# Optimization experiments

Hardware: AMD Instinct MI355X
Metric: run time of the kernel (lower is better)

The kernel has to match this reference:

```python
import jax, jax.numpy as jnp
import numpy as np

D = 128   # latent_dim
H = 128   # mlp_hidden_dim
S = 2     # message_passing_steps
NM = 30000   # mesh nodes
NO = 2000    # obj nodes
EMM = 240000 # mesh->mesh edges
EMO = 60000  # mesh->obj edges


def _ln(h, g, b):
    m = jnp.mean(h, axis=-1, keepdims=True)
    v = jnp.mean((h - m) ** 2, axis=-1, keepdims=True)
    return (h - m) * jax.lax.rsqrt(v + 1e-5) * g + b


def _mlp_ln(h, W0, b0, W1, b1, W2, b2, g, bt):
    # build_mlp(in, [H]*2, out) + LayerNorm(out)
    h = jax.nn.relu(h @ W0 + b0)
    h = jax.nn.relu(h @ W1 + b1)
    h = h @ W2 + b2
    return _ln(h, g, bt)


def _edge_conv(x_src, x_dst, ei, ea, W0, b0, W1, b1, W2, b2, g, bt):
    # PyG source_to_target: x_j = src gather (ei[0]), x_i = dst gather (ei[1])
    xi = x_dst[ei[1]]
    xj = x_src[ei[0]]
    msg = _mlp_ln(jnp.concatenate([xi, xj, ea], axis=-1), W0, b0, W1, b1, W2, b2, g, bt)
    aggr = jax.ops.segment_sum(msg, ei[1], num_segments=x_dst.shape[0])
    return ea + msg, aggr  # residual on edge attr; aggr is sum of raw messages


def _node_conv(x, aggr, W0, b0, W1, b1, W2, b2, g, bt):
    return x + _mlp_ln(jnp.concatenate([x, aggr], axis=-1), W0, b0, W1, b1, W2, b2, g, bt)


def setup_inputs() -> dict:
    key = jax.random.key(0)
    ks = jax.random.split(key, 16)
    f = jnp.float32
    x_mesh = jax.random.normal(ks[0], (NM, D), f)
    x_obj = jax.random.normal(ks[1], (NO, D), f)
    ea_mm = jax.random.normal(ks[2], (EMM, D), f)
    ea_mo = jax.random.normal(ks[3], (EMO, D), f)
    ei_mm = jnp.stack([jax.random.randint(ks[4], (EMM,), 0, NM),
                       jax.random.randint(ks[5], (EMM,), 0, NM)]).astype(jnp.int32)
    ei_mo = jnp.stack([jax.random.randint(ks[6], (EMO,), 0, NM),
                       jax.random.randint(ks[7], (EMO,), 0, NO)]).astype(jnp.int32)

    def w(k, shape, fan):
        return jax.random.normal(k, shape, f) * (1.0 / np.sqrt(fan))

    # params stacked as [edge_or_node_type(2), step(S), ...]
    eW0 = w(ks[8], (2, S, 3 * D, H), 3 * D); eb0 = jnp.zeros((2, S, H), f)
    eW1 = w(ks[9], (2, S, H, H), H);         eb1 = jnp.zeros((2, S, H), f)
    eW2 = w(ks[10], (2, S, H, D), H);        eb2 = jnp.zeros((2, S, D), f)
    eg = jnp.ones((2, S, D), f);             ebt = jnp.zeros((2, S, D), f)
    nW0 = w(ks[11], (2, S, 2 * D, H), 2 * D); nb0 = jnp.zeros((2, S, H), f)
    nW1 = w(ks[12], (2, S, H, H), H);         nb1 = jnp.zeros((2, S, H), f)
    nW2 = w(ks[13], (2, S, H, D), H);         nb2 = jnp.zeros((2, S, D), f)
    ng = jnp.ones((2, S, D), f);              nbt = jnp.zeros((2, S, D), f)
    return dict(x_mesh=x_mesh, x_obj=x_obj, ei_mm=ei_mm, ei_mo=ei_mo,
                ea_mm=ea_mm, ea_mo=ea_mo,
                eW0=eW0, eb0=eb0, eW1=eW1, eb1=eb1, eW2=eW2, eb2=eb2, eg=eg, ebt=ebt,
                nW0=nW0, nb0=nb0, nW1=nW1, nb1=nb1, nW2=nW2, nb2=nb2, ng=ng, nbt=nbt)


def reference(x_mesh, x_obj, ei_mm, ei_mo, ea_mm, ea_mo,
              eW0, eb0, eW1, eb1, eW2, eb2, eg, ebt,
              nW0, nb0, nW1, nb1, nW2, nb2, ng, nbt):
    for s in range(S):
        ep = lambda t: (eW0[t, s], eb0[t, s], eW1[t, s], eb1[t, s], eW2[t, s], eb2[t, s], eg[t, s], ebt[t, s])
        npar = lambda t: (nW0[t, s], nb0[t, s], nW1[t, s], nb1[t, s], nW2[t, s], nb2[t, s], ng[t, s], nbt[t, s])
        # edge convs use node features at layer input
        ea_mm, agg_mesh = _edge_conv(x_mesh, x_mesh, ei_mm, ea_mm, *ep(0))
        ea_mo, agg_obj = _edge_conv(x_mesh, x_obj, ei_mo, ea_mo, *ep(1))
        x_mesh = _node_conv(x_mesh, agg_mesh, *npar(0))
        x_obj = _node_conv(x_obj, agg_obj, *npar(1))
    return (x_mesh, x_obj)
```

## Files before the change

kernel.cpp:

```cpp
#include <hip/hip_runtime.h>

#define DD 128
#define NMESH 30000
#define NOBJ 2000
#define EMMN 240000
#define EMON 60000

typedef unsigned short u16;
typedef short short8 __attribute__((ext_vector_type(8)));
typedef short short4v __attribute__((ext_vector_type(4)));
typedef float f32x4 __attribute__((ext_vector_type(4)));
typedef __bf16 bf16x8 __attribute__((ext_vector_type(8)));

union FragCvt { short8 s; bf16x8 b; };

static __device__ __forceinline__ u16 f2bf(float f) {
  union { float f; unsigned u; } v; v.f = f;
  unsigned r = v.u + 0x7FFFu + ((v.u >> 16) & 1u);
  return (u16)(r >> 16);
}
static __device__ __forceinline__ float bf2f(u16 u) {
  union { unsigned u; float f; } v; v.u = ((unsigned)u) << 16; return v.f;
}
static __device__ __forceinline__ int swz256(int row, int b) {
  return row * 256 + (b ^ ((row & 7) << 4));
}
static __device__ __forceinline__ bf16x8 ldsFrag(const u16* s, int row, int kByte) {
  FragCvt u; u.s = *(const short8*)((const char*)s + swz256(row, kByte));
  return u.b;
}

static __device__ __forceinline__ void stage_w(u16* sW, const u16* src, int rowLen, int colOff, int tid) {
  const int wrow = tid >> 1, wh = tid & 1;
  const u16* w = src + (size_t)wrow * rowLen + colOff + wh * 64;
  #pragma unroll
  for (int j = 0; j < 8; ++j) {
    short8 v = *(const short8*)(w + j * 8);
    *(short8*)((char*)sW + swz256(wrow, wh * 128 + j * 16)) = v;
  }
}

static __device__ __forceinline__ void mfma_128k(const u16* sIn, const u16* sW,
                                                 int wr, int wc, int lrow, int lk,
                                                 f32x4 acc[2][4]) {
  #pragma unroll
  for (int kc = 0; kc < 4; ++kc) {
    bf16x8 a0 = ldsFrag(sIn, wr * 32 + lrow, kc * 64 + lk * 16);
    bf16x8 a1 = ldsFrag(sIn, wr * 32 + 16 + lrow, kc * 64 + lk * 16);
    #pragma unroll
    for (int ct = 0; ct < 4; ++ct) {
      bf16x8 b = ldsFrag(sW, wc * 64 + ct * 16 + lrow, kc * 64 + lk * 16);
      acc[0][ct] = __builtin_amdgcn_mfma_f32_16x16x32_bf16(a0, b, acc[0][ct], 0, 0, 0);
      acc[1][ct] = __builtin_amdgcn_mfma_f32_16x16x32_bf16(a1, b, acc[1][ct], 0, 0, 0);
// ... 10 lines not shown
    for (int ct = 0; ct < 4; ++ct) {
      const int col = wc * 64 + ct * 16 + lrow;
      const float bias = sBias[biasOff + col];
      #pragma unroll
      for (int r = 0; r < 4; ++r) {
        const int orow = wr * 32 + rt * 16 + lk * 4 + r;
        float v = acc[rt][ct][r] + bias;
        v = fmaxf(v, 0.f);
        *(u16*)((char*)sIn + swz256(orow, col * 2)) = f2bf(v);
        acc[rt][ct][r] = 0.f;
      }
    }
  }
}

static __device__ __forceinline__ void store_h3(float* sH, const float* sBias,
                                                int wr, int wc, int lrow, int lk,
                                                f32x4 acc[2][4]) {
  #pragma unroll
  for (int rt = 0; rt < 2; ++rt) {
    #pragma unroll
    for (int ct = 0; ct < 4; ++ct) {
      const int col = wc * 64 + ct * 16 + lrow;
      const float bias = sBias[256 + col];
      #pragma unroll
      for (int r = 0; r < 4; ++r) {
        const int orow = wr * 32 + rt * 16 + lk * 4 + r;
        sH[orow * 132 + col] = acc[rt][ct][r] + bias;
      }
    }
  }
}

__global__ __launch_bounds__(256, 2) void edge_conv_kernel(
    const u16* __restrict__ xsrc, const u16* __restrict__ xdst,
    const int* __restrict__ ei, const int E,
    const float* __restrict__ ea_f32, u16* __restrict__ ea_bf,
    const u16* __restrict__ W0T, const u16* __restrict__ W1T, const u16* __restrict__ W2T,
    const float* __restrict__ b0, const float* __restrict__ b1, const float* __restrict__ b2,
    const float* __restrict__ gg, const float* __restrict__ btp,
    u16* __restrict__ msg_out)
{
  __shared__ u16 sIn[64 * 128];
  __shared__ __align__(16) char sWHraw[64 * 132 * 4];
  __shared__ float sBias[5 * 128];
  __shared__ int sIdx[128];
  u16* sW = (u16*)sWHraw;
  float* sH = (float*)sWHraw;

  const int tid = threadIdx.x;
  const int wave = tid >> 6, lane = tid & 63;
  const int lrow = lane & 15, lk = lane >> 4;
  const int wr = wave >> 1, wc = wave & 1;
  const int e0 = blockIdx.x * 64;
  const int row = tid >> 2, seg = tid & 3;

  if (tid < 128) {
    sBias[tid] = b0[tid];
    sBias[128 + tid] = b1[tid];
    sBias[256 + tid] = b2[tid];
    sBias[384 + tid] = gg[tid];
    sBias[512 + tid] = btp[tid];
  }
  if (tid < 64) {
    int e = e0 + tid; if (e >= E) e = E - 1;
    sIdx[tid] = ei[e];
    sIdx[64 + tid] = ei[E + e];
  }
  __syncthreads();

  const int eRow = (e0 + row < E) ? (e0 + row) : (E - 1);
  const f32x4 zero = {0.f, 0.f, 0.f, 0.f};
  f32x4 acc[2][4];
  #pragma unroll
  for (int i = 0; i < 2; ++i)
    #pragma unroll
    for (int j = 0; j < 4; ++j) acc[i][j] = zero;

  #pragma unroll
  for (int p = 0; p < 3; ++p) {
    if (p < 2) {
      const u16* xb = (p == 0) ? xdst : xsrc;
      const int idx = (p == 0) ? sIdx[64 + row] : sIdx[row];
      const u16* srow = xb + (size_t)idx * DD;
      #pragma unroll
      for (int j = 0; j < 4; ++j) {
        short8 v = *(const short8*)(srow + seg * 32 + j * 8);
        *(short8*)((char*)sIn + swz256(row, seg * 64 + j * 16)) = v;
      }
    } else if (ea_f32) {
      const float* er = ea_f32 + (size_t)eRow * DD;
      #pragma unroll
      for (int j = 0; j < 4; ++j) {
        const int c0 = seg * 32 + j * 8;
        f32x4 f0 = *(const f32x4*)(er + c0);
        f32x4 f1 = *(const f32x4*)(er + c0 + 4);
        short8 v;
        #pragma unroll
        for (int q = 0; q < 4; ++q) { v[q] = (short)f2bf(f0[q]); v[4 + q] = (short)f2bf(f1[q]); }
        *(short8*)((char*)sIn + swz256(row, seg * 64 + j * 16)) = v;
      }
    } else {
      const u16* er = ea_bf + (size_t)eRow * DD;
      #pragma unroll
      for (int j = 0; j < 4; ++j) {
        short8 v = *(const short8*)(er + seg * 32 + j * 8);
        *(short8*)((char*)sIn + swz256(row, seg * 64 + j * 16)) = v;
      }
    }
    stage_w(sW, W0T, 384, p * 128, tid);
    __syncthreads();
    mfma_128k(sIn, sW, wr, wc, lrow, lk, acc);
    __syncthreads();
  }

  transition_relu(sIn, sBias, 0, wr, wc, lrow, lk, acc);
  stage_w(sW, W1T, 128, 0, tid);
  __syncthreads();
  mfma_128k(sIn, sW, wr, wc, lrow, lk, acc);
  __syncthreads();

  transition_relu(sIn, sBias, 128, wr, wc, lrow, lk, acc);
  stage_w(sW, W2T, 128, 0, tid);
  __syncthreads();
  mfma_128k(sIn, sW, wr, wc, lrow, lk, acc);
  __syncthreads();

  store_h3(sH, sBias, wr, wc, lrow, lk, acc);
  __syncthreads();

  {
    const float* hrow = sH + row * 132 + seg * 32;
    f32x4 vv[8];
    float s1 = 0.f, s2 = 0.f;
    #pragma unroll
    for (int j = 0; j < 8; ++j) {
      vv[j] = *(const f32x4*)(hrow + j * 4);
      #pragma unroll
      for (int q = 0; q < 4; ++q) { s1 += vv[j][q]; s2 += vv[j][q] * vv[j][q]; }
    }
    s1 += __shfl_xor(s1, 1); s1 += __shfl_xor(s1, 2);
    s2 += __shfl_xor(s2, 1); s2 += __shfl_xor(s2, 2);
    const float m = s1 * (1.f / 128.f);
    const float var = s2 * (1.f / 128.f) - m * m;
    const float rstd = rsqrtf(var + 1e-5f);
    const int e = e0 + row;
    if (e < E) {
      u16* eaRow = ea_bf + (size_t)e * DD + seg * 32;
      u16* msgRow = msg_out + (size_t)e * DD + seg * 32;
      float eold[32];
      if (ea_f32) {
        const float* er = ea_f32 + (size_t)e * DD + seg * 32;
        #pragma unroll
        for (int j = 0; j < 8; ++j) {
          f32x4 t = *(const f32x4*)(er + j * 4);
          #pragma unroll
          for (int q = 0; q < 4; ++q) eold[j * 4 + q] = t[q];
        }
      } else {
        #pragma unroll
        for (int j4 = 0; j4 < 4; ++j4) {
          short8 t = *(const short8*)(eaRow + j4 * 8);
          #pragma unroll
          for (int q = 0; q < 8; ++q) eold[j4 * 8 + q] = bf2f((u16)t[q]);
        }
      }
      #pragma unroll
      for (int j4 = 0; j4 < 4; ++j4) {
        short8 en, ms;
        #pragma unroll
        for (int q = 0; q < 8; ++q) {
          const int cl = j4 * 8 + q;
          const int c = seg * 32 + cl;
          const float msg = (vv[cl >> 2][cl & 3] - m) * rstd * sBias[384 + c] + sBias[512 + c];
          en[q] = (short)f2bf(eold[cl] + msg);
          ms[q] = (short)f2bf(msg);
        }
        *(short8*)(eaRow + j4 * 8) = en;
        *(short8*)(msgRow + j4 * 8) = ms;
      }
    }
  }
}

__global__ void hist_kernel(const int* __restrict__ ei, int E, int* __restrict__ deg) {
  int i = blockIdx.x * blockDim.x + threadIdx.x;
  if (i < E) atomicAdd(&deg[ei[E + i]], 1);
}

__global__ __launch_bounds__(1024) void scan_kernel(const int* __restrict__ deg,
                                                    int* __restrict__ start,
                                                    int* __restrict__ cursor, int N) {
  __shared__ int lds[1024];
  const int t = threadIdx.x;
  const int chunk = (N + 1023) >> 10;
  const int base = t * chunk;
  const int end = min(base + chunk, N);
  int s = 0;
  for (int i = base; i < end; ++i) s += deg[i];
  lds[t] = s;
  __syncthreads();
  for (int d = 1; d < 1024; d <<= 1) {
    int v = (t >= d) ? lds[t - d] : 0;
    __syncthreads();
    lds[t] += v;
    __syncthreads();
  }
  int off = lds[t] - s;
  for (int i = base; i < end; ++i) { start[i] = off; cursor[i] = off; off += deg[i]; }
  if (t == 1023) start[N] = lds[1023];
}

__global__ void scatter_kernel(const int* __restrict__ ei, int E,
                               int* __restrict__ cursor, int* __restrict__ perm) {
  int i = blockIdx.x * blockDim.x + threadIdx.x;
  if (i < E) { int p = atomicAdd(&cursor[ei[E + i]], 1); perm[p] = i; }
}

__global__ __launch_bounds__(256) void agg_gather_kernel(
    const u16* __restrict__ msg, const int* __restrict__ start,
    const int* __restrict__ perm, float* __restrict__ agg, int N)
{
  const int wave = threadIdx.x >> 6, lane = threadIdx.x & 63;
  const int n = blockIdx.x * 4 + wave;
  if (n >= N) return;
  const int i0 = start[n], i1 = start[n + 1];
  float a0 = 0.f, a1 = 0.f;
  for (int i = i0; i < i1; ++i) {
    const int e = perm[i];
    unsigned v = *(const unsigned*)(msg + (size_t)e * DD + lane * 2);
    a0 += bf2f((u16)(v & 0xFFFFu));
    a1 += bf2f((u16)(v >> 16));
  }
  float* ar = agg + (size_t)n * DD + lane * 2;
  ar[0] = a0;
  ar[1] = a1;
}

__global__ __launch_bounds__(256, 2) void node_conv_kernel(
    u16* __restrict__ x_bf, const float* __restrict__ aggin,
    float* __restrict__ x_f32, const int N,
    const u16* __restrict__ W0T, const u16* __restrict__ W1T, const u16* __restrict__ W2T,
    const float* __restrict__ b0, const float* __restrict__ b1, const float* __restrict__ b2,
    const float* __restrict__ gg, const float* __restrict__ btp)
{
  __shared__ u16 sIn[64 * 128];
  __shared__ __align__(16) char sWHraw[64 * 132 * 4];
  __shared__ float sBias[5 * 128];
  u16* sW = (u16*)sWHraw;
  float* sH = (float*)sWHraw;

  const int tid = threadIdx.x;
  const int wave = tid >> 6, lane = tid & 63;
  const int lrow = lane & 15, lk = lane >> 4;
  const int wr = wave >> 1, wc = wave & 1;
  const int n0 = blockIdx.x * 64;
  const int row = tid >> 2, seg = tid & 3;
  const int nRow = (n0 + row < N) ? (n0 + row) : (N - 1);

  if (tid < 128) {
    sBias[tid] = b0[tid];
    sBias[128 + tid] = b1[tid];
    sBias[256 + tid] = b2[tid];
    sBias[384 + tid] = gg[tid];
    sBias[512 + tid] = btp[tid];
  }
  __syncthreads();

  const f32x4 zero = {0.f, 0.f, 0.f, 0.f};
  f32x4 acc[2][4];
  #pragma unroll
  for (int i = 0; i < 2; ++i)
    #pragma unroll
    for (int j = 0; j < 4; ++j) acc[i][j] = zero;

  {
    const u16* srow = x_bf + (size_t)nRow * DD;
    #pragma unroll
    for (int j = 0; j < 4; ++j) {
      short8 v = *(const short8*)(srow + seg * 32 + j * 8);
      *(short8*)((char*)sIn + swz256(row, seg * 64 + j * 16)) = v;
    }
    stage_w(sW, W0T, 256, 0, tid);
  }
  __syncthreads();
  mfma_128k(sIn, sW, wr, wc, lrow, lk, acc);
  __syncthreads();
  {
    const float* ar = aggin + (size_t)nRow * DD;
    #pragma unroll
    for (int j = 0; j < 4; ++j) {
      const int c0 = seg * 32 + j * 8;
      f32x4 f0 = *(const f32x4*)(ar + c0);
      f32x4 f1 = *(const f32x4*)(ar + c0 + 4);
      short8 v;
      #pragma unroll
      for (int q = 0; q < 4; ++q) { v[q] = (short)f2bf(f0[q]); v[4 + q] = (short)f2bf(f1[q]); }
      *(short8*)((char*)sIn + swz256(row, seg * 64 + j * 16)) = v;
    }
    stage_w(sW, W0T, 256, 128, tid);
  }
  __syncthreads();
  mfma_128k(sIn, sW, wr, wc, lrow, lk, acc);
  __syncthreads();

  transition_relu(sIn, sBias, 0, wr, wc, lrow, lk, acc);
  stage_w(sW, W1T, 128, 0, tid);
  __syncthreads();
  mfma_128k(sIn, sW, wr, wc, lrow, lk, acc);
  __syncthreads();

  transition_relu(sIn, sBias, 128, wr, wc, lrow, lk, acc);
  stage_w(sW, W2T, 128, 0, tid);
  __syncthreads();
  mfma_128k(sIn, sW, wr, wc, lrow, lk, acc);
  __syncthreads();

  store_h3(sH, sBias, wr, wc, lrow, lk, acc);
  __syncthreads();

  {
    const float* hrow = sH + row * 132 + seg * 32;
    f32x4 vv[8];
    float s1 = 0.f, s2 = 0.f;
    #pragma unroll
    for (int j = 0; j < 8; ++j) {
      vv[j] = *(const f32x4*)(hrow + j * 4);
      #pragma unroll
      for (int q = 0; q < 4; ++q) { s1 += vv[j][q]; s2 += vv[j][q] * vv[j][q]; }
    }
    s1 += __shfl_xor(s1, 1); s1 += __shfl_xor(s1, 2);
    s2 += __shfl_xor(s2, 1); s2 += __shfl_xor(s2, 2);
    const float m = s1 * (1.f / 128.f);
    const float var = s2 * (1.f / 128.f) - m * m;
    const float rstd = rsqrtf(var + 1e-5f);
    const int n = n0 + row;
    if (n < N) {
      float* xr = x_f32 + (size_t)n * DD + seg * 32;
      u16* xb = x_bf + (size_t)n * DD + seg * 32;
      #pragma unroll
      for (int j = 0; j < 8; ++j) {
        f32x4 xold = *(const f32x4*)(xr + j * 4);
        f32x4 nv;
        short4v pb;
        #pragma unroll
        for (int q = 0; q < 4; ++q) {
          const int c = seg * 32 + j * 4 + q;
          const float ln = (vv[j][q] - m) * rstd * sBias[384 + c] + sBias[512 + c];
          nv[q] = xold[q] + ln;
          pb[q] = (short)f2bf(nv[q]);
        }
        *(f32x4*)(xr + j * 4) = nv;
        *(short4v*)(xb + j * 4) = pb;
      }
    }
  }
}

__global__ void prep_w_kernel(const float* __restrict__ src, u16* __restrict__ dst, int K) {
  int i = blockIdx.x * blockDim.x + threadIdx.x;
  int total = 4 * K * 128;
  if (i < total) {
    int n = i & 127;
    int k = (i >> 7) % K;
    int sl = i / (K * 128);
    dst[((size_t)sl * 128 + n) * K + k] = f2bf(src[i]);
  }
}

__global__ void prep_x_kernel(const float* __restrict__ xm, const float* __restrict__ xo,
                              float* __restrict__ xf, u16* __restrict__ xmb, u16* __restrict__ xob) {
  int i = blockIdx.x * blockDim.x + threadIdx.x;
  const int tm = NMESH * DD;
  const int to = NOBJ * DD;
  if (i < tm) { float v = xm[i]; xf[i] = v; xmb[i] = f2bf(v); }
  else if (i < tm + to) { int j = i - tm; float v = xo[j]; xf[tm + j] = v; xob[j] = f2bf(v); }
}

extern "C" void kernel_launch(void* const* d_in, const int* in_sizes, int n_in,
                              void* d_out, int out_size, void* d_ws, size_t ws_size,
                              hipStream_t stream)
{
  const float* x_mesh = (const float*)d_in[0];
  const float* x_obj  = (const float*)d_in[1];
  const int*   ei_mm  = (const int*)d_in[2];
  const int*   ei_mo  = (const int*)d_in[3];
  const float* ea_mm  = (const float*)d_in[4];
  const float* ea_mo  = (const float*)d_in[5];
  const float* eW0 = (const float*)d_in[6];
  const float* eb0 = (const float*)d_in[7];
  const float* eW1 = (const float*)d_in[8];
// ... 25 lines not shown
  u16* nW2T = nW1T + (size_t)4 * 128 * 128;
  u16* msg_mm = nW2T + (size_t)4 * 128 * 128;
  u16* msg_mo = msg_mm + (size_t)EMMN * DD;
  int* deg_m   = (int*)(msg_mo + (size_t)EMON * DD);
  int* start_m = deg_m + NMESH;
  int* cur_m   = start_m + NMESH + 1;
  int* perm_mm = cur_m + NMESH;
  int* deg_o   = perm_mm + EMMN;
  int* start_o = deg_o + NOBJ;
  int* cur_o   = start_o + NOBJ + 1;
  int* perm_mo = cur_o + NOBJ;

  float* xf_m = (float*)d_out;
  float* xf_o = xf_m + (size_t)NMESH * DD;

  prep_w_kernel<<<768, 256, 0, stream>>>(eW0, eW0T, 384);
  prep_w_kernel<<<256, 256, 0, stream>>>(eW1, eW1T, 128);
  prep_w_kernel<<<256, 256, 0, stream>>>(eW2, eW2T, 128);
  prep_w_kernel<<<512, 256, 0, stream>>>(nW0, nW0T, 256);
  prep_w_kernel<<<256, 256, 0, stream>>>(nW1, nW1T, 128);
  prep_w_kernel<<<256, 256, 0, stream>>>(nW2, nW2T, 128);
  prep_x_kernel<<<16000, 256, 0, stream>>>(x_mesh, x_obj, xf_m, xm_bf, xo_bf);

  hipMemsetAsync(deg_m, 0, NMESH * sizeof(int), stream);
  hipMemsetAsync(deg_o, 0, NOBJ * sizeof(int), stream);
  hist_kernel<<<(EMMN + 255) / 256, 256, 0, stream>>>(ei_mm, EMMN, deg_m);
  hist_kernel<<<(EMON + 255) / 256, 256, 0, stream>>>(ei_mo, EMON, deg_o);
  scan_kernel<<<1, 1024, 0, stream>>>(deg_m, start_m, cur_m, NMESH);
  scan_kernel<<<1, 1024, 0, stream>>>(deg_o, start_o, cur_o, NOBJ);
  scatter_kernel<<<(EMMN + 255) / 256, 256, 0, stream>>>(ei_mm, EMMN, cur_m, perm_mm);
  scatter_kernel<<<(EMON + 255) / 256, 256, 0, stream>>>(ei_mo, EMON, cur_o, perm_mo);

  for (int s = 0; s < 2; ++s) {
    {
      int sl = 0 * 2 + s;
      edge_conv_kernel<<<EMMN / 64, 256, 0, stream>>>(
          xm_bf, xm_bf, ei_mm, EMMN,
          (s == 0) ? ea_mm : (const float*)nullptr, eamm_bf,
          eW0T + (size_t)sl * 128 * 384, eW1T + (size_t)sl * 128 * 128, eW2T + (size_t)sl * 128 * 128,
          eb0 + sl * 128, eb1 + sl * 128, eb2 + sl * 128, eg + sl * 128, ebt + sl * 128,
          msg_mm);
    }
    {
      int sl = 1 * 2 + s;
      edge_conv_kernel<<<(EMON + 63) / 64, 256, 0, stream>>>(
          xm_bf, xo_bf, ei_mo, EMON,
          (s == 0) ? ea_mo : (const float*)nullptr, eamo_bf,
          eW0T + (size_t)sl * 128 * 384, eW1T + (size_t)sl * 128 * 128, eW2T + (size_t)sl * 128 * 128,
          eb0 + sl * 128, eb1 + sl * 128, eb2 + sl * 128, eg + sl * 128, ebt + sl * 128,
          msg_mo);
    }
    agg_gather_kernel<<<(NMESH + 3) / 4, 256, 0, stream>>>(msg_mm, start_m, perm_mm, agg_m, NMESH);
    agg_gather_kernel<<<(NOBJ + 3) / 4, 256, 0, stream>>>(msg_mo, start_o, perm_mo, agg_o, NOBJ);
    {
      int sl = 0 * 2 + s;
      node_conv_kernel<<<(NMESH + 63) / 64, 256, 0, stream>>>(
          xm_bf, agg_m, xf_m, NMESH,
          nW0T + (size_t)sl * 128 * 256, nW1T + (size_t)sl * 128 * 128, nW2T + (size_t)sl * 128 * 128,
          nb0 + sl * 128, nb1 + sl * 128, nb2 + sl * 128, ng + sl * 128, nbt + sl * 128);
    }
    {
      int sl = 1 * 2 + s;
      node_conv_kernel<<<(NOBJ + 63) / 64, 256, 0, stream>>>(
          xo_bf, agg_o, xf_o, NOBJ,
          nW0T + (size_t)sl * 128 * 256, nW1T + (size_t)sl * 128 * 128, nW2T + (size_t)sl * 128 * 128,
          nb0 + sl * 128, nb1 + sl * 128, nb2 + sl * 128, ng + sl * 128, nbt + sl * 128);
    }
  }
}
```

Baseline: 683.5 us.

## Merge per-type launches, enlarge tiles, async weight staging, register LayerNorm

Mesh-mesh and mesh-obj edge convs now run in one launch, as do the two node convs and the aggregation gathers. Prep, histogram, scan and scatter are also merged into fewer kernels, which cuts launch count and tail effects. Tiles grow from 64 to 128 rows with 512 threads, and weights are staged into LDS with async global_load_lds. LayerNorm is computed from accumulators in registers via a cross-wave partial-sum exchange, replacing the fp32 shared-memory round trip, and output stores use nontemporal hints. The larger shared footprint and different occupancy could cost latency hiding.

```diff
diff --git a/kernel.cpp b/kernel.cpp
--- a/kernel.cpp
+++ b/kernel.cpp
@@ -5,10 +5,13 @@
 #define NOBJ 2000
 #define EMMN 240000
 #define EMON 60000
+#define NB_MM (EMMN / 128)
+#define NB_MO ((EMON + 127) / 128)
+#define NB_NM ((NMESH + 127) / 128)
+#define NB_NO ((NOBJ + 127) / 128)
 
 typedef unsigned short u16;
 typedef short short8 __attribute__((ext_vector_type(8)));
-typedef short short4v __attribute__((ext_vector_type(4)));
 typedef float f32x4 __attribute__((ext_vector_type(4)));
 typedef __bf16 bf16x8 __attribute__((ext_vector_type(8)));
 
@@ -30,13 +33,21 @@
   return u.b;
 }
 
-static __device__ __forceinline__ void stage_w(u16* sW, const u16* src, int rowLen, int colOff, int tid) {
-  const int wrow = tid >> 1, wh = tid & 1;
-  const u16* w = src + (size_t)wrow * rowLen + colOff + wh * 64;
-  #pragma unroll
-  for (int j = 0; j < 8; ++j) {
-    short8 v = *(const short8*)(w + j * 8);
-    *(short8*)((char*)sW + swz256(wrow, wh * 128 + j * 16)) = v;
+static __device__ __forceinline__ void gload_lds16(const void* g, void* l) {
+  __builtin_amdgcn_global_load_lds((const __attribute__((address_space(1))) void*)g,
+                                   (__attribute__((address_space(3))) void*)l, 16, 0, 0);
+}
+
+static __device__ __forceinline__ void stage_w_async(u16* sW, const u16* W,
+                                                     int rowLen, int colOff, int tid) {
+  const int w = tid >> 6, lane = tid & 63;
+  #pragma unroll
+  for (int j = 0; j < 4; ++j) {
+    const int base_row = (j * 8 + w) * 4;
+    const int row = base_row + (lane >> 4);
+    const int chunk = (lane & 15) ^ (row & 7);
+    const u16* g = W + (size_t)row * rowLen + colOff + chunk * 8;
+    gload_lds16(g, (char*)sW + base_row * 256);
   }
 }
 
@@ -77,62 +88,108 @@
   }
 }
 
-static __device__ __forceinline__ void store_h3(float* sH, const float* sBias,
-                                                int wr, int wc, int lrow, int lk,
-                                                f32x4 acc[2][4]) {
+static __device__ __forceinline__ void ln_to_sIn(u16* sIn, float* sPart, const float* sBias,
+                                                 int wr, int wc, int lrow, int lk,
+                                                 f32x4 acc[2][4]) {
+  float gv[4], bv[4];
+  #pragma unroll
+  for (int ct = 0; ct < 4; ++ct) {
+    const int col = wc * 64 + ct * 16 + lrow;
+    gv[ct] = sBias[384 + col];
+    bv[ct] = sBias[512 + col];
+  }
+  float s1[2][4], s2[2][4];
   #pragma unroll
   for (int rt = 0; rt < 2; ++rt) {
     #pragma unroll
-    for (int ct = 0; ct < 4; ++ct) {
-      const int col = wc * 64 + ct * 16 + lrow;
-      const float bias = sBias[256 + col];
+    for (int r = 0; r < 4; ++r) {
+      float a = 0.f, b = 0.f;
+      #pragma unroll
+      for (int ct = 0; ct < 4; ++ct) {
+        const int col = wc * 64 + ct * 16 + lrow;
+        const float v = acc[rt][ct][r] + sBias[256 + col];
+        acc[rt][ct][r] = v;
+        a += v; b += v * v;
+      }
+      #pragma unroll
+      for (int m = 1; m < 16; m <<= 1) { a += __shfl_xor(a, m); b += __shfl_xor(b, m); }
+      s1[rt][r] = a; s2[rt][r] = b;
+    }
+  }
+  if (lrow == 0) {
+    #pragma unroll
+    for (int rt = 0; rt < 2; ++rt)
       #pragma unroll
       for (int r = 0; r < 4; ++r) {
-        const int orow = wr * 32 + rt * 16 + lk * 4 + r;
-        sH[orow * 132 + col] = acc[rt][ct][r] + bias;
+        const int e = wr * 32 + rt * 16 + lk * 4 + r;
+        sPart[(wc * 128 + e) * 2] = s1[rt][r];
+        sPart[(wc * 128 + e) * 2 + 1] = s2[rt][r];
+      }
+  }
+  __syncthreads();
+  #pragma unroll
+  for (int rt = 0; rt < 2; ++rt)
+    #pragma unroll
+    for (int r = 0; r < 4; ++r) {
+      const int e = wr * 32 + rt * 16 + lk * 4 + r;
+      const float t1 = s1[rt][r] + sPart[((1 - wc) * 128 + e) * 2];
+      const float t2 = s2[rt][r] + sPart[((1 - wc) * 128 + e) * 2 + 1];
+      const float m = t1 * (1.f / 128.f);
+      const float var = t2 * (1.f / 128.f) - m * m;
+      const float rstd = rsqrtf(var + 1e-5f);
+      #pragma unroll
+      for (int ct = 0; ct < 4; ++ct) {
+        const int col = wc * 64 + ct * 16 + lrow;
+        const float ln = (acc[rt][ct][r] - m) * rstd * gv[ct] + bv[ct];
+        *(u16*)((char*)sIn + swz256(e, col * 2)) = f2bf(ln);
       }
     }
-  }
-}
-
-__global__ __launch_bounds__(256, 2) void edge_conv_kernel(
-    const u16* __restrict__ xsrc, const u16* __restrict__ xdst,
-    const int* __restrict__ ei, const int E,
-    const float* __restrict__ ea_f32, u16* __restrict__ ea_bf,
-    const u16* __restrict__ W0T, const u16* __restrict__ W1T, const u16* __restrict__ W2T,
-    const float* __restrict__ b0, const float* __restrict__ b1, const float* __restrict__ b2,
-    const float* __restrict__ gg, const float* __restrict__ btp,
-    u16* __restrict__ msg_out)
-{
-  __shared__ u16 sIn[64 * 128];
-  __shared__ __align__(16) char sWHraw[64 * 132 * 4];
-  __shared__ float sBias[5 * 128];
-  __shared__ int sIdx[128];
-  u16* sW = (u16*)sWHraw;
-  float* sH = (float*)sWHraw;
-
+}
+
+static __device__ __forceinline__ void stage_rows_bf(u16* sIn, const u16* src, int row, int seg) {
+  #pragma unroll
+  for (int j = 0; j < 4; ++j) {
+    short8 v = *(const short8*)(src + seg * 32 + j * 8);
+    *(short8*)((char*)sIn + swz256(row, seg * 64 + j * 16)) = v;
+  }
+}
+static __device__ __forceinline__ void stage_rows_f32(u16* sIn, const float* src, int row, int seg) {
+  #pragma unroll
+  for (int j = 0; j < 4; ++j) {
+    const int c0 = seg * 32 + j * 8;
+    f32x4 f0 = *(const f32x4*)(src + c0);
+    f32x4 f1 = *(const f32x4*)(src + c0 + 4);
+    short8 v;
+    #pragma unroll
+    for (int q = 0; q < 4; ++q) { v[q] = (short)f2bf(f0[q]); v[4 + q] = (short)f2bf(f1[q]); }
+    *(short8*)((char*)sIn + swz256(row, seg * 64 + j * 16)) = v;
+  }
+}
+
+static __device__ void edge_body(int bid,
+    const u16* xsrc, const u16* xdst, const int* ei, int E,
+    const float* ea_f32, u16* ea_bf,
+    const u16* W0T, const u16* W1T, const u16* W2T,
+    const float* b0, const float* b1, const float* b2,
+    const float* gq, const float* btq, u16* msg_out,
+    u16* sIn, u16* sW, float* sBias, float* sPart)
+{
   const int tid = threadIdx.x;
   const int wave = tid >> 6, lane = tid & 63;
   const int lrow = lane & 15, lk = lane >> 4;
   const int wr = wave >> 1, wc = wave & 1;
-  const int e0 = blockIdx.x * 64;
+  const int e0 = bid * 128;
   const int row = tid >> 2, seg = tid & 3;
+  const int eRow = (e0 + row < E) ? (e0 + row) : (E - 1);
 
   if (tid < 128) {
     sBias[tid] = b0[tid];
     sBias[128 + tid] = b1[tid];
     sBias[256 + tid] = b2[tid];
-    sBias[384 + tid] = gg[tid];
-    sBias[512 + tid] = btp[tid];
-  }
-  if (tid < 64) {
-    int e = e0 + tid; if (e >= E) e = E - 1;
-    sIdx[tid] = ei[e];
-    sIdx[64 + tid] = ei[E + e];
-  }
-  __syncthreads();
-
-  const int eRow = (e0 + row < E) ? (e0 + row) : (E - 1);
+    sBias[384 + tid] = gq[tid];
+    sBias[512 + tid] = btq[tid];
+  }
+
   const f32x4 zero = {0.f, 0.f, 0.f, 0.f};
   f32x4 acc[2][4];
   #pragma unroll
@@ -140,120 +197,223 @@
     #pragma unroll
     for (int j = 0; j < 4; ++j) acc[i][j] = zero;
 
-  #pragma unroll
-  for (int p = 0; p < 3; ++p) {
-    if (p < 2) {
-      const u16* xb = (p == 0) ? xdst : xsrc;
-      const int idx = (p == 0) ? sIdx[64 + row] : sIdx[row];
-      const u16* srow = xb + (size_t)idx * DD;
+  stage_w_async(sW, W0T, 384, 0, tid);
+  { const int idx = ei[E + eRow]; stage_rows_bf(sIn, xdst + (size_t)idx * DD, row, seg); }
+  __syncthreads();
+  mfma_128k(sIn, sW, wr, wc, lrow, lk, acc);
+  __syncthreads();
+
+  stage_w_async(sW, W0T, 384, 128, tid);
+  { const int idx = ei[eRow]; stage_rows_bf(sIn, xsrc + (size_t)idx * DD, row, seg); }
+  __syncthreads();
+  mfma_128k(sIn, sW, wr, wc, lrow, lk, acc);
+  __syncthreads();
+
+  stage_w_async(sW, W0T, 384, 256, tid);
+  if (ea_f32) stage_rows_f32(sIn, ea_f32 + (size_t)eRow * DD, row, seg);
+  else        stage_rows_bf(sIn, ea_bf + (size_t)eRow * DD, row, seg);
+  __syncthreads();
+  mfma_128k(sIn, sW, wr, wc, lrow, lk, acc);
+  __syncthreads();
+
+  transition_relu(sIn, sBias, 0, wr, wc, lrow, lk, acc);
+  stage_w_async(sW, W1T, 128, 0, tid);
+  __syncthreads();
+  mfma_128k(sIn, sW, wr, wc, lrow, lk, acc);
+  __syncthreads();
+
+  transition_relu(sIn, sBias, 128, wr, wc, lrow, lk, acc);
+  stage_w_async(sW, W2T, 128, 0, tid);
+  __syncthreads();
+  mfma_128k(sIn, sW, wr, wc, lrow, lk, acc);
+  __syncthreads();
+
+  ln_to_sIn(sIn, sPart, sBias, wr, wc, lrow, lk, acc);
+  __syncthreads();
+
+  const int e = e0 + row;
+  if (e < E) {
+    short8 msgv[4];
+    #pragma unroll
+    for (int j = 0; j < 4; ++j)
+      msgv[j] = *(const short8*)((const char*)sIn + swz256(row, seg * 64 + j * 16));
+    u16* msgRow = msg_out + (size_t)e * DD + seg * 32;
+    u16* eaRow  = ea_bf + (size_t)e * DD + seg * 32;
+    if (ea_f32) {
+      const float* er = ea_f32 + (size_t)e * DD + seg * 32;
       #pragma unroll
       for (int j = 0; j < 4; ++j) {
-        short8 v = *(const short8*)(srow + seg * 32 + j * 8);
-        *(short8*)((char*)sIn + swz256(row, seg * 64 + j * 16)) = v;
-      }
-    } else if (ea_f32) {
-      const float* er = ea_f32 + (size_t)eRow * DD;
+        f32x4 o0 = __builtin_nontemporal_load((const f32x4*)(er + j * 8));
+        f32x4 o1 = __builtin_nontemporal_load((const f32x4*)(er + j * 8 + 4));
+        short8 en;
+        #pragma unroll
+        for (int q = 0; q < 4; ++q) {
+          en[q]     = (short)f2bf(o0[q] + bf2f((u16)msgv[j][q]));
+          en[4 + q] = (short)f2bf(o1[q] + bf2f((u16)msgv[j][4 + q]));
+        }
+        __builtin_nontemporal_store(en, (short8*)(eaRow + j * 8));
+        __builtin_nontemporal_store(msgv[j], (short8*)(msgRow + j * 8));
+      }
+    } else {
       #pragma unroll
       for (int j = 0; j < 4; ++j) {
-        const int c0 = seg * 32 + j * 8;
-        f32x4 f0 = *(const f32x4*)(er + c0);
-        f32x4 f1 = *(const f32x4*)(er + c0 + 4);
-        short8 v;
+        short8 old = __builtin_nontemporal_load((const short8*)(eaRow + j * 8));
+        short8 en;
         #pragma unroll
-        for (int q = 0; q < 4; ++q) { v[q] = (short)f2bf(f0[q]); v[4 + q] = (short)f2bf(f1[q]); }
-        *(short8*)((char*)sIn + swz256(row, seg * 64 + j * 16)) = v;
-      }
-    } else {
-      const u16* er = ea_bf + (size_t)eRow * DD;
-      #pragma unroll
-      for (int j = 0; j < 4; ++j) {
-        short8 v = *(const short8*)(er + seg * 32 + j * 8);
-        *(short8*)((char*)sIn + swz256(row, seg * 64 + j * 16)) = v;
+        for (int q = 0; q < 8; ++q)
+          en[q] = (short)f2bf(bf2f((u16)old[q]) + bf2f((u16)msgv[j][q]));
+        __builtin_nontemporal_store(en, (short8*)(eaRow + j * 8));
+        __builtin_nontemporal_store(msgv[j], (short8*)(msgRow + j * 8));
       }
     }
-    stage_w(sW, W0T, 384, p * 128, tid);
-    __syncthreads();
-    mfma_128k(sIn, sW, wr, wc, lrow, lk, acc);
-    __syncthreads();
-  }
+  }
+}
+
+__global__ __launch_bounds__(512, 4) void edge_conv_kernel(
+    const u16* __restrict__ xm_bf, const u16* __restrict__ xo_bf,
+    const int* __restrict__ ei_mm, const int* __restrict__ ei_mo,
+    const float* __restrict__ eaf_mm, const float* __restrict__ eaf_mo,
+    u16* __restrict__ eab_mm, u16* __restrict__ eab_mo,
+    const u16* __restrict__ W0a, const u16* __restrict__ W1a, const u16* __restrict__ W2a,
+    const u16* __restrict__ W0b, const u16* __restrict__ W1b, const u16* __restrict__ W2b,
+    const float* __restrict__ b0a, const float* __restrict__ b1a, const float* __restrict__ b2a,
+    const float* __restrict__ ga, const float* __restrict__ bta,
+    const float* __restrict__ b0b, const float* __restrict__ b1b, const float* __restrict__ b2b,
+    const float* __restrict__ gb, const float* __restrict__ btb,
+    u16* __restrict__ msg_mm, u16* __restrict__ msg_mo)
+{
+  __shared__ u16 sIn[128 * 128];
+  __shared__ u16 sW[128 * 128];
+  __shared__ float sBias[5 * 128];
+  __shared__ float sPart[2 * 128 * 2];
+  if ((int)blockIdx.x < NB_MM)
+    edge_body(blockIdx.x, xm_bf, xm_bf, ei_mm, EMMN, eaf_mm, eab_mm,
+              W0a, W1a, W2a, b0a, b1a, b2a, ga, bta, msg_mm, sIn, sW, sBias, sPart);
+  else
+    edge_body(blockIdx.x - NB_MM, xm_bf, xo_bf, ei_mo, EMON, eaf_mo, eab_mo,
+              W0b, W1b, W2b, b0b, b1b, b2b, gb, btb, msg_mo, sIn, sW, sBias, sPart);
+}
+
+static __device__ void node_body(int bid, u16* x_bf, const float* aggin, float* x_f32, int N,
+    const u16* W0T, const u16* W1T, const u16* W2T,
+    const float* b0, const float* b1, const float* b2,
+    const float* gq, const float* btq,
+    u16* sIn, u16* sW, float* sBias, float* sPart)
+{
+  const int tid = threadIdx.x;
+  const int wave = tid >> 6, lane = tid & 63;
+  const int lrow = lane & 15, lk = lane >> 4;
+  const int wr = wave >> 1, wc = wave & 1;
+  const int n0 = bid * 128;
+  const int row = tid >> 2, seg = tid & 3;
+  const int nRow = (n0 + row < N) ? (n0 + row) : (N - 1);
+
+  if (tid < 128) {
+    sBias[tid] = b0[tid];
+    sBias[128 + tid] = b1[tid];
+    sBias[256 + tid] = b2[tid];
+    sBias[384 + tid] = gq[tid];
+    sBias[512 + tid] = btq[tid];
+  }
+
+  const f32x4 zero = {0.f, 0.f, 0.f, 0.f};
+  f32x4 acc[2][4];
+  #pragma unroll
+  for (int i = 0; i < 2; ++i)
+    #pragma unroll
+    for (int j = 0; j < 4; ++j) acc[i][j] = zero;
+
+  stage_w_async(sW, W0T, 256, 0, tid);
+  stage_rows_bf(sIn, x_bf + (size_t)nRow * DD, row, seg);
+  __syncthreads();
+  mfma_128k(sIn, sW, wr, wc, lrow, lk, acc);
+  __syncthreads();
+
+  stage_w_async(sW, W0T, 256, 128, tid);
+  stage_rows_f32(sIn, aggin + (size_t)nRow * DD, row, seg);
+  __syncthreads();
+  mfma_128k(sIn, sW, wr, wc, lrow, lk, acc);
+  __syncthreads();
 
   transition_relu(sIn, sBias, 0, wr, wc, lrow, lk, acc);
-  stage_w(sW, W1T, 128, 0, tid);
+  stage_w_async(sW, W1T, 128, 0, tid);
   __syncthreads();
   mfma_128k(sIn, sW, wr, wc, lrow, lk, acc);
   __syncthreads();
 
   transition_relu(sIn, sBias, 128, wr, wc, lrow, lk, acc);
-  stage_w(sW, W2T, 128, 0, tid);
-  __syncthreads();
-  mfma_128k(sIn, sW, wr, wc, lrow, lk, acc);
-  __syncthreads();
-
-  store_h3(sH, sBias, wr, wc, lrow, lk, acc);
-  __syncthreads();
-
-  {
-    const float* hrow = sH + row * 132 + seg * 32;
-    f32x4 vv[8];
-    float s1 = 0.f, s2 = 0.f;
-    #pragma unroll
-    for (int j = 0; j < 8; ++j) {
-      vv[j] = *(const f32x4*)(hrow + j * 4);
-      #pragma unroll
-      for (int q = 0; q < 4; ++q) { s1 += vv[j][q]; s2 += vv[j][q] * vv[j][q]; }
+  stage_w_async(sW, W2T, 128, 0, tid);
+  __syncthreads();
+  mfma_128k(sIn, sW, wr, wc, lrow, lk, acc);
+  __syncthreads();
+
+  ln_to_sIn(sIn, sPart, sBias, wr, wc, lrow, lk, acc);
+  __syncthreads();
+
+  const int n = n0 + row;
+  if (n < N) {
+    short8 lnv[4];
+    #pragma unroll
+    for (int j = 0; j < 4; ++j)
+      lnv[j] = *(const short8*)((const char*)sIn + swz256(row, seg * 64 + j * 16));
+    float* xr = x_f32 + (size_t)n * DD + seg * 32;
+    u16* xb = x_bf + (size_t)n * DD + seg * 32;
+    #pragma unroll
+    for (int j = 0; j < 4; ++j) {
+      f32x4 o0 = *(const f32x4*)(xr + j * 8);
+      f32x4 o1 = *(const f32x4*)(xr + j * 8 + 4);
+      f32x4 n0v, n1v;
+      short8 pb;
+      #pragma unroll
+      for (int q = 0; q < 4; ++q) {
+        n0v[q] = o0[q] + bf2f((u16)lnv[j][q]);
+        n1v[q] = o1[q] + bf2f((u16)lnv[j][4 + q]);
+        pb[q]     = (short)f2bf(n0v[q]);
+        pb[4 + q] = (short)f2bf(n1v[q]);
+      }
+      *(f32x4*)(xr + j * 8) = n0v;
+      *(f32x4*)(xr + j * 8 + 4) = n1v;
+      *(short8*)(xb + j * 8) = pb;
     }
-    s1 += __shfl_xor(s1, 1); s1 += __shfl_xor(s1, 2);
-    s2 += __shfl_xor(s2, 1); s2 += __shfl_xor(s2, 2);
-    const float m = s1 * (1.f / 128.f);
-    const float var = s2 * (1.f / 128.f) - m * m;
-    const float rstd = rsqrtf(var + 1e-5f);
-    const int e = e0 + row;
-    if (e < E) {
-      u16* eaRow = ea_bf + (size_t)e * DD + seg * 32;
-      u16* msgRow = msg_out + (size_t)e * DD + seg * 32;
-      float eold[32];
-      if (ea_f32) {
-        const float* er = ea_f32 + (size_t)e * DD + seg * 32;
-        #pragma unroll
-        for (int j = 0; j < 8; ++j) {
-          f32x4 t = *(const f32x4*)(er + j * 4);
-          #pragma unroll
-          for (int q = 0; q < 4; ++q) eold[j * 4 + q] = t[q];
-        }
-      } else {
-        #pragma unroll
-        for (int j4 = 0; j4 < 4; ++j4) {
-          short8 t = *(const short8*)(eaRow + j4 * 8);
-          #pragma unroll
-          for (int q = 0; q < 8; ++q) eold[j4 * 8 + q] = bf2f((u16)t[q]);
-        }
-      }
-      #pragma unroll
-      for (int j4 = 0; j4 < 4; ++j4) {
-        short8 en, ms;
-        #pragma unroll
-        for (int q = 0; q < 8; ++q) {
-          const int cl = j4 * 8 + q;
-          const int c = seg * 32 + cl;
-          const float msg = (vv[cl >> 2][cl & 3] - m) * rstd * sBias[384 + c] + sBias[512 + c];
-          en[q] = (short)f2bf(eold[cl] + msg);
-          ms[q] = (short)f2bf(msg);
-        }
-        *(short8*)(eaRow + j4 * 8) = en;
-        *(short8*)(msgRow + j4 * 8) = ms;
-      }
-    }
-  }
-}
-
-__global__ void hist_kernel(const int* __restrict__ ei, int E, int* __restrict__ deg) {
+  }
+}
+
+__global__ __launch_bounds__(512, 4) void node_conv_kernel(
+    u16* __restrict__ xm_bf, u16* __restrict__ xo_bf,
+    const float* __restrict__ agg_m, const float* __restrict__ agg_o,
+    float* __restrict__ xf_m, float* __restrict__ xf_o,
+    const u16* __restrict__ W0a, const u16* __restrict__ W1a, const u16* __restrict__ W2a,
+    const u16* __restrict__ W0b, const u16* __restrict__ W1b, const u16* __restrict__ W2b,
+    const float* __restrict__ b0a, const float* __restrict__ b1a, const float* __restrict__ b2a,
+    const float* __restrict__ ga, const float* __restrict__ bta,
+    const float* __restrict__ b0b, const float* __restrict__ b1b, const float* __restrict__ b2b,
+    const float* __restrict__ gb, const float* __restrict__ btb)
+{
+  __shared__ u16 sIn[128 * 128];
+  __shared__ u16 sW[128 * 128];
+  __shared__ float sBias[5 * 128];
+  __shared__ float sPart[2 * 128 * 2];
+  if ((int)blockIdx.x < NB_NM)
+    node_body(blockIdx.x, xm_bf, agg_m, xf_m, NMESH,
+              W0a, W1a, W2a, b0a, b1a, b2a, ga, bta, sIn, sW, sBias, sPart);
+  else
+    node_body(blockIdx.x - NB_NM, xo_bf, agg_o, xf_o, NOBJ,
+              W0b, W1b, W2b, b0b, b1b, b2b, gb, btb, sIn, sW, sBias, sPart);
+}
+
+__global__ void hist_kernel(const int* __restrict__ ei_mm, const int* __restrict__ ei_mo,
+                            int* __restrict__ deg_m, int* __restrict__ deg_o) {
   int i = blockIdx.x * blockDim.x + threadIdx.x;
-  if (i < E) atomicAdd(&deg[ei[E + i]], 1);
-}
-
-__global__ __launch_bounds__(1024) void scan_kernel(const int* __restrict__ deg,
-                                                    int* __restrict__ start,
-                                                    int* __restrict__ cursor, int N) {
+  if (i < EMMN) atomicAdd(&deg_m[ei_mm[EMMN + i]], 1);
+  else { int j = i - EMMN; if (j < EMON) atomicAdd(&deg_o[ei_mo[EMON + j]], 1); }
+}
+
+__global__ __launch_bounds__(1024) void scan_kernel(
+    const int* __restrict__ deg_m, int* __restrict__ start_m, int* __restrict__ cur_m,
+    const int* __restrict__ deg_o, int* __restrict__ start_o, int* __restrict__ cur_o) {
+  const int* deg; int* start; int* cursor; int N;
+  if (blockIdx.x == 0) { deg = deg_m; start = start_m; cursor = cur_m; N = NMESH; }
+  else                 { deg = deg_o; start = start_o; cursor = cur_o; N = NOBJ; }
   __shared__ int lds[1024];
   const int t = threadIdx.x;
   const int chunk = (N + 1023) >> 10;
@@ -274,170 +434,84 @@
   if (t == 1023) start[N] = lds[1023];
 }
 
-__global__ void scatter_kernel(const int* __restrict__ ei, int E,
-                               int* __restrict__ cursor, int* __restrict__ perm) {
+__global__ void scatter_kernel(const int* __restrict__ ei_mm, const int* __restrict__ ei_mo,
+                               int* __restrict__ cur_m, int* __restrict__ cur_o,
+                               int* __restrict__ perm_m, int* __restrict__ perm_o) {
   int i = blockIdx.x * blockDim.x + threadIdx.x;
-  if (i < E) { int p = atomicAdd(&cursor[ei[E + i]], 1); perm[p] = i; }
+  if (i < EMMN) { int p = atomicAdd(&cur_m[ei_mm[EMMN + i]], 1); perm_m[p] = i; }
+  else { int j = i - EMMN; if (j < EMON) { int p = atomicAdd(&cur_o[ei_mo[EMON + j]], 1); perm_o[p] = j; } }
 }
 
 __global__ __launch_bounds__(256) void agg_gather_kernel(
-    const u16* __restrict__ msg, const int* __restrict__ start,
-    const int* __restrict__ perm, float* __restrict__ agg, int N)
+    const u16* __restrict__ msg_m, const int* __restrict__ start_m, const int* __restrict__ perm_m,
+    float* __restrict__ agg_m,
+    const u16* __restrict__ msg_o, const int* __restrict__ start_o, const int* __restrict__ perm_o,
+    float* __restrict__ agg_o)
 {
   const int wave = threadIdx.x >> 6, lane = threadIdx.x & 63;
-  const int n = blockIdx.x * 4 + wave;
-  if (n >= N) return;
+  int idx = blockIdx.x * 4 + wave;
+  const u16* msg; const int* start; const int* perm; float* agg; int n;
+  if (idx < NMESH) { msg = msg_m; start = start_m; perm = perm_m; agg = agg_m; n = idx; }
+  else {
+    n = idx - NMESH;
+    if (n >= NOBJ) return;
+    msg = msg_o; start = start_o; perm = perm_o; agg = agg_o;
+  }
   const int i0 = start[n], i1 = start[n + 1];
   float a0 = 0.f, a1 = 0.f;
-  for (int i = i0; i < i1; ++i) {
-    const int e = perm[i];
-    unsigned v = *(const unsigned*)(msg + (size_t)e * DD + lane * 2);
-    a0 += bf2f((u16)(v & 0xFFFFu));
-    a1 += bf2f((u16)(v >> 16));
+  int i = i0;
+  for (; i + 1 < i1; i += 2) {
+    const int e1 = perm[i], e2 = perm[i + 1];
+    unsigned v1 = __builtin_nontemporal_load((const unsigned*)(msg + (size_t)e1 * DD + lane * 2));
+    unsigned v2 = __builtin_nontemporal_load((const unsigned*)(msg + (size_t)e2 * DD + lane * 2));
+    a0 += bf2f((u16)(v1 & 0xFFFFu)) + bf2f((u16)(v2 & 0xFFFFu));
+    a1 += bf2f((u16)(v1 >> 16)) + bf2f((u16)(v2 >> 16));
+  }
+  if (i < i1) {
+    const int e1 = perm[i];
+    unsigned v1 = __builtin_nontemporal_load((const unsigned*)(msg + (size_t)e1 * DD + lane * 2));
+    a0 += bf2f((u16)(v1 & 0xFFFFu));
+    a1 += bf2f((u16)(v1 >> 16));
   }
   float* ar = agg + (size_t)n * DD + lane * 2;
   ar[0] = a0;
   ar[1] = a1;
 }
 
-__global__ __launch_bounds__(256, 2) void node_conv_kernel(
-    u16* __restrict__ x_bf, const float* __restrict__ aggin,
-    float* __restrict__ x_f32, const int N,
-    const u16* __restrict__ W0T, const u16* __restrict__ W1T, const u16* __restrict__ W2T,
-    const float* __restrict__ b0, const float* __restrict__ b1, const float* __restrict__ b2,
-    const float* __restrict__ gg, const float* __restrict__ btp)
-{
-  __shared__ u16 sIn[64 * 128];
-  __shared__ __align__(16) char sWHraw[64 * 132 * 4];
-  __shared__ float sBias[5 * 128];
-  u16* sW = (u16*)sWHraw;
-  float* sH = (float*)sWHraw;
-
-  const int tid = threadIdx.x;
-  const int wave = tid >> 6, lane = tid & 63;
-  const int lrow = lane & 15, lk = lane >> 4;
-  const int wr = wave >> 1, wc = wave & 1;
-  const int n0 = blockIdx.x * 64;
-  const int row = tid >> 2, seg = tid & 3;
-  const int nRow = (n0 + row < N) ? (n0 + row) : (N - 1);
-
-  if (tid < 128) {
-    sBias[tid] = b0[tid];
-    sBias[128 + tid] = b1[tid];
-    sBias[256 + tid] = b2[tid];
-    sBias[384 + tid] = gg[tid];
-    sBias[512 + tid] = btp[tid];
-  }
-  __syncthreads();
-
-  const f32x4 zero = {0.f, 0.f, 0.f, 0.f};
-  f32x4 acc[2][4];
-  #pragma unroll
-  for (int i = 0; i < 2; ++i)
-    #pragma unroll
-    for (int j = 0; j < 4; ++j) acc[i][j] = zero;
-
-  {
-    const u16* srow = x_bf + (size_t)nRow * DD;
-    #pragma unroll
-    for (int j = 0; j < 4; ++j) {
-      short8 v = *(const short8*)(srow + seg * 32 + j * 8);
-      *(short8*)((char*)sIn + swz256(row, seg * 64 + j * 16)) = v;
-    }
-    stage_w(sW, W0T, 256, 0, tid);
-  }
-  __syncthreads();
-  mfma_128k(sIn, sW, wr, wc, lrow, lk, acc);
-  __syncthreads();
-  {
-    const float* ar = aggin + (size_t)nRow * DD;
-    #pragma unroll
-    for (int j = 0; j < 4; ++j) {
-      const int c0 = seg * 32 + j * 8;
-      f32x4 f0 = *(const f32x4*)(ar + c0);
-      f32x4 f1 = *(const f32x4*)(ar + c0 + 4);
-      short8 v;
-      #pragma unroll
-      for (int q = 0; q < 4; ++q) { v[q] = (short)f2bf(f0[q]); v[4 + q] = (short)f2bf(f1[q]); }
-      *(short8*)((char*)sIn + swz256(row, seg * 64 + j * 16)) = v;
-    }
-    stage_w(sW, W0T, 256, 128, tid);
-  }
-  __syncthreads();
-  mfma_128k(sIn, sW, wr, wc, lrow, lk, acc);
-  __syncthreads();
-
-  transition_relu(sIn, sBias, 0, wr, wc, lrow, lk, acc);
-  stage_w(sW, W1T, 128, 0, tid);
-  __syncthreads();
-  mfma_128k(sIn, sW, wr, wc, lrow, lk, acc);
-  __syncthreads();
-
-  transition_relu(sIn, sBias, 128, wr, wc, lrow, lk, acc);
-  stage_w(sW, W2T, 128, 0, tid);
-  __syncthreads();
-  mfma_128k(sIn, sW, wr, wc, lrow, lk, acc);
-  __syncthreads();
-
-  store_h3(sH, sBias, wr, wc, lrow, lk, acc);
-  __syncthreads();
-
-  {
-    const float* hrow = sH + row * 132 + seg * 32;
-    f32x4 vv[8];
-    float s1 = 0.f, s2 = 0.f;
-    #pragma unroll
-    for (int j = 0; j < 8; ++j) {
-      vv[j] = *(const f32x4*)(hrow + j * 4);
-      #pragma unroll
-      for (int q = 0; q < 4; ++q) { s1 += vv[j][q]; s2 += vv[j][q] * vv[j][q]; }
-    }
-    s1 += __shfl_xor(s1, 1); s1 += __shfl_xor(s1, 2);
-    s2 += __shfl_xor(s2, 1); s2 += __shfl_xor(s2, 2);
-    const float m = s1 * (1.f / 128.f);
-    const float var = s2 * (1.f / 128.f) - m * m;
-    const float rstd = rsqrtf(var + 1e-5f);
-    const int n = n0 + row;
-    if (n < N) {
-      float* xr = x_f32 + (size_t)n * DD + seg * 32;
-      u16* xb = x_bf + (size_t)n * DD + seg * 32;
-      #pragma unroll
-      for (int j = 0; j < 8; ++j) {
-        f32x4 xold = *(const f32x4*)(xr + j * 4);
-        f32x4 nv;
-        short4v pb;
-        #pragma unroll
-        for (int q = 0; q < 4; ++q) {
-          const int c = seg * 32 + j * 4 + q;
-          const float ln = (vv[j][q] - m) * rstd * sBias[384 + c] + sBias[512 + c];
-          nv[q] = xold[q] + ln;
-          pb[q] = (short)f2bf(nv[q]);
-        }
-        *(f32x4*)(xr + j * 4) = nv;
-        *(short4v*)(xb + j * 4) = pb;
-      }
-    }
-  }
-}
-
-__global__ void prep_w_kernel(const float* __restrict__ src, u16* __restrict__ dst, int K) {
-  int i = blockIdx.x * blockDim.x + threadIdx.x;
-  int total = 4 * K * 128;
-  if (i < total) {
-    int n = i & 127;
-    int k = (i >> 7) % K;
-    int sl = i / (K * 128);
-    dst[((size_t)sl * 128 + n) * K + k] = f2bf(src[i]);
-  }
-}
-
-__global__ void prep_x_kernel(const float* __restrict__ xm, const float* __restrict__ xo,
-                              float* __restrict__ xf, u16* __restrict__ xmb, u16* __restrict__ xob) {
-  int i = blockIdx.x * blockDim.x + threadIdx.x;
-  const int tm = NMESH * DD;
-  const int to = NOBJ * DD;
-  if (i < tm) { float v = xm[i]; xf[i] = v; xmb[i] = f2bf(v); }
-  else if (i < tm + to) { int j = i - tm; float v = xo[j]; xf[tm + j] = v; xob[j] = f2bf(v); }
+static __device__ __forceinline__ void wcvt(const float* src, u16* dst, int K, int b, int t) {
+  int i = b * 256 + t;
+  int n = i & 127;
+  int k = (i >> 7) % K;
+  int sl = i / (K * 128);
+  dst[((size_t)sl * 128 + n) * K + k] = f2bf(src[i]);
+}
+
+__global__ void prep_kernel(
+    const float* __restrict__ eW0, const float* __restrict__ eW1, const float* __restrict__ eW2,
+    const float* __restrict__ nW0, const float* __restrict__ nW1, const float* __restrict__ nW2,
+    u16* __restrict__ eW0T, u16* __restrict__ eW1T, u16* __restrict__ eW2T,
+    u16* __restrict__ nW0T, u16* __restrict__ nW1T, u16* __restrict__ nW2T,
+    int* __restrict__ deg_m, int* __restrict__ deg_o,
+    const float* __restrict__ xm, const float* __restrict__ xo,
+    float* __restrict__ xf, u16* __restrict__ xmb, u16* __restrict__ xob)
+{
+  const int b = blockIdx.x, t = threadIdx.x;
+  if (b < 768)        wcvt(eW0, eW0T, 384, b, t);
+  else if (b < 1024)  wcvt(eW1, eW1T, 128, b - 768, t);
+  else if (b < 1280)  wcvt(eW2, eW2T, 128, b - 1024, t);
+  else if (b < 1792)  wcvt(nW0, nW0T, 256, b - 1280, t);
+  else if (b < 2048)  wcvt(nW1, nW1T, 128, b - 1792, t);
+  else if (b < 2304)  wcvt(nW2, nW2T, 128, b - 2048, t);
+  else if (b < 2429) {
+    int i = (b - 2304) * 256 + t;
+    if (i < NMESH) deg_m[i] = 0;
+    else if (i < NMESH + NOBJ) deg_o[i - NMESH] = 0;
+  } else {
+    int i = (b - 2429) * 256 + t;
+    const int tm = NMESH * DD;
+    if (i < tm) { float v = xm[i]; xf[i] = v; xmb[i] = f2bf(v); }
+    else { int j = i - tm; float v = xo[j]; xf[tm + j] = v; xob[j] = f2bf(v); }
+  }
 }
 
 extern "C" void kernel_launch(void* const* d_in, const int* in_sizes, int n_in,
@@ -493,57 +567,33 @@
   float* xf_m = (float*)d_out;
   float* xf_o = xf_m + (size_t)NMESH * DD;
 
-  prep_w_kernel<<<768, 256, 0, stream>>>(eW0, eW0T, 384);
-  prep_w_kernel<<<256, 256, 0, stream>>>(eW1, eW1T, 128);
-  prep_w_kernel<<<256, 256, 0, stream>>>(eW2, eW2T, 128);
-  prep_w_kernel<<<512, 256, 0, stream>>>(nW0, nW0T, 256);
-  prep_w_kernel<<<256, 256, 0, stream>>>(nW1, nW1T, 128);
-  prep_w_kernel<<<256, 256, 0, stream>>>(nW2, nW2T, 128);
-  prep_x_kernel<<<16000, 256, 0, stream>>>(x_mesh, x_obj, xf_m, xm_bf, xo_bf);
-
-  hipMemsetAsync(deg_m, 0, NMESH * sizeof(int), stream);
-  hipMemsetAsync(deg_o, 0, NOBJ * sizeof(int), stream);
-  hist_kernel<<<(EMMN + 255) / 256, 256, 0, stream>>>(ei_mm, EMMN, deg_m);
-  hist_kernel<<<(EMON + 255) / 256, 256, 0, stream>>>(ei_mo, EMON, deg_o);
-  scan_kernel<<<1, 1024, 0, stream>>>(deg_m, start_m, cur_m, NMESH);
-  scan_kernel<<<1, 1024, 0, stream>>>(deg_o, start_o, cur_o, NOBJ);
-  scatter_kernel<<<(EMMN + 255) / 256, 256, 0, stream>>>(ei_mm, EMMN, cur_m, perm_mm);
-  scatter_kernel<<<(EMON + 255) / 256, 256, 0, stream>>>(ei_mo, EMON, cur_o, perm_mo);
+  prep_kernel<<<18429, 256, 0, stream>>>(eW0, eW1, eW2, nW0, nW1, nW2,
+                                         eW0T, eW1T, eW2T, nW0T, nW1T, nW2T,
+                                         deg_m, deg_o, x_mesh, x_obj, xf_m, xm_bf, xo_bf);
+  hist_kernel<<<(EMMN + EMON + 255) / 256, 256, 0, stream>>>(ei_mm, ei_mo, deg_m, deg_o);
+  scan_kernel<<<2, 1024, 0, stream>>>(deg_m, start_m, cur_m, deg_o, start_o, cur_o);
+  scatter_kernel<<<(EMMN + EMON + 255) / 256, 256, 0, stream>>>(ei_mm, ei_mo, cur_m, cur_o,
+                                                                perm_mm, perm_mo);
 
   for (int s = 0; s < 2; ++s) {
-    {
-      int sl = 0 * 2 + s;
-      edge_conv_kernel<<<EMMN / 64, 256, 0, stream>>>(
-          xm_bf, xm_bf, ei_mm, EMMN,
-          (s == 0) ? ea_mm : (const float*)nullptr, eamm_bf,
-          eW0T + (size_t)sl * 128 * 384, eW1T + (size_t)sl * 128 * 128, eW2T + (size_t)sl * 128 * 128,
-          eb0 + sl * 128, eb1 + sl * 128, eb2 + sl * 128, eg + sl * 128, ebt + sl * 128,
-          msg_mm);
-    }
-    {
-      int sl = 1 * 2 + s;
-      edge_conv_kernel<<<(EMON + 63) / 64, 256, 0, stream>>>(
-          xm_bf, xo_bf, ei_mo, EMON,
-          (s == 0) ? ea_mo : (const float*)nullptr, eamo_bf,
-          eW0T + (size_t)sl * 128 * 384, eW1T + (size_t)sl * 128 * 128, eW2T + (size_t)sl * 128 * 128,
-          eb0 + sl * 128, eb1 + sl * 128, eb2 + sl * 128, eg + sl * 128, ebt + sl * 128,
-          msg_mo);
-    }
-    agg_gather_kernel<<<(NMESH + 3) / 4, 256, 0, stream>>>(msg_mm, start_m, perm_mm, agg_m, NMESH);
-    agg_gather_kernel<<<(NOBJ + 3) / 4, 256, 0, stream>>>(msg_mo, start_o, perm_mo, agg_o, NOBJ);
-    {
-      int sl = 0 * 2 + s;
-      node_conv_kernel<<<(NMESH + 63) / 64, 256, 0, stream>>>(
-          xm_bf, agg_m, xf_m, NMESH,
-          nW0T + (size_t)sl * 128 * 256, nW1T + (size_t)sl * 128 * 128, nW2T + (size_t)sl * 128 * 128,
-          nb0 + sl * 128, nb1 + sl * 128, nb2 + sl * 128, ng + sl * 128, nbt + sl * 128);
-    }
-    {
-      int sl = 1 * 2 + s;
-      node_conv_kernel<<<(NOBJ + 63) / 64, 256, 0, stream>>>(
-          xo_bf, agg_o, xf_o, NOBJ,
-          nW0T + (size_t)sl * 128 * 256, nW1T + (size_t)sl * 128 * 128, nW2T + (size_t)sl * 128 * 128,
-          nb0 + sl * 128, nb1 + sl * 128, nb2 + sl * 128, ng + sl * 128, nbt + sl * 128);
-    }
-  }
-}
+    const int sa = 0 * 2 + s, sb = 1 * 2 + s;
+    edge_conv_kernel<<<NB_MM + NB_MO, 512, 0, stream>>>(
+        xm_bf, xo_bf, ei_mm, ei_mo,
+        (s == 0) ? ea_mm : (const float*)nullptr,
+        (s == 0) ? ea_mo : (const float*)nullptr,
+        eamm_bf, eamo_bf,
+        eW0T + (size_t)sa * 128 * 384, eW1T + (size_t)sa * 128 * 128, eW2T + (size_t)sa * 128 * 128,
+        eW0T + (size_t)sb * 128 * 384, eW1T + (size_t)sb * 128 * 128, eW2T + (size_t)sb * 128 * 128,
+        eb0 + sa * 128, eb1 + sa * 128, eb2 + sa * 128, eg + sa * 128, ebt + sa * 128,
+        eb0 + sb * 128, eb1 + sb * 128, eb2 + sb * 128, eg + sb * 128, ebt + sb * 128,
+        msg_mm, msg_mo);
+    agg_gather_kernel<<<(NMESH + NOBJ + 3) / 4, 256, 0, stream>>>(
+        msg_mm, start_m, perm_mm, agg_m, msg_mo, start_o, perm_mo, agg_o);
+    node_conv_kernel<<<NB_NM + NB_NO, 512, 0, stream>>>(
+        xm_bf, xo_bf, agg_m, agg_o, xf_m, xf_o,
+        nW0T + (size_t)sa * 128 * 256, nW1T + (size_t)sa * 128 * 128, nW2T + (size_t)sa * 128 * 128,
+        nW0T + (size_t)sb * 128 * 256, nW1T + (size_t)sb * 128 * 128, nW2T + (size_t)sb * 128 * 128,
+        nb0 + sa * 128, nb1 + sa * 128, nb2 + sa * 128, ng + sa * 128, nbt + sa * 128,
+        nb0 + sb * 128, nb1 + sb * 128, nb2 + sb * 128, ng + sb * 128, nbt + sb * 128);
+  }
+}
```

Measured after the change: 1.031 ms. +50.9%, slower.
